# Performance work log

Measured on AMD Instinct MI355X. Metric: run time of the kernel, lower is better.

Reference implementation:

```python
import jax, jax.numpy as jnp
import numpy as np

DIM = 4096
N_HEADS = 32
N_KV = 8
HEAD_DIM = 128
BATCH = 32
CACHE_LEN = 2048 + 128  # hard-coded in init_kv_cache
START_POS = 2047
ROPE_BASE = 10000.0


def setup_inputs() -> dict:
    key = jax.random.key(0)
    ks = jax.random.split(key, 5)
    qkv_dim = (N_HEADS + 2 * N_KV) * HEAD_DIM  # fused QKV width
    return {
        "x": jax.random.normal(ks[0], (BATCH, DIM), jnp.float32) * 0.02,
        "wqkv": jax.random.normal(ks[1], (DIM, qkv_dim), jnp.float32) * 0.02,
        "wo": jax.random.normal(ks[2], (DIM, DIM), jnp.float32) * 0.02,
        "cache_k": jax.random.normal(ks[3], (BATCH, N_KV, CACHE_LEN, HEAD_DIM), jnp.float32) * 0.02,
        "cache_v": jax.random.normal(ks[4], (BATCH, N_KV, CACHE_LEN, HEAD_DIM), jnp.float32) * 0.02,
        "start_pos": START_POS,
    }


def _rope_cos_sin(pos):
    # Llama half-split RoPE; equivalent to the head_dim x head_dim rotation matrix
    half = HEAD_DIM // 2
    inv_freq = 1.0 / (ROPE_BASE ** (jnp.arange(half, dtype=jnp.float32) * 2.0 / HEAD_DIM))
    ang = pos * inv_freq
    cos = jnp.concatenate([jnp.cos(ang), jnp.cos(ang)])
    sin = jnp.concatenate([jnp.sin(ang), jnp.sin(ang)])
    return cos, sin


def _rotate_half(t):
    h = t.shape[-1] // 2
    return jnp.concatenate([-t[..., h:], t[..., :h]], axis=-1)


def reference(x, wqkv, wo, cache_k, cache_v, start_pos):
    scale = 1.0 / np.sqrt(HEAD_DIM)
    n_rep = N_HEADS // N_KV

    # fused QKV projection
    qkv = x @ wqkv  # (B, (H + 2*K) * D)
    q = qkv[:, : N_HEADS * HEAD_DIM].reshape(BATCH, N_KV, n_rep, HEAD_DIM)
    k = qkv[:, N_HEADS * HEAD_DIM : (N_HEADS + N_KV) * HEAD_DIM].reshape(BATCH, N_KV, HEAD_DIM)
    v = qkv[:, (N_HEADS + N_KV) * HEAD_DIM :].reshape(BATCH, N_KV, HEAD_DIM)

    # RoPE at position start_pos (rotation-matrix form in the original)
    cos, sin = _rope_cos_sin(jnp.float32(start_pos))
    q = q * cos + _rotate_half(q) * sin
    k = k * cos + _rotate_half(k) * sin

    # KV cache update at start_pos
    cache_k = cache_k.at[:, :, start_pos, :].set(k)
    cache_v = cache_v.at[:, :, start_pos, :].set(v)

    # grouped-query attention over the whole (masked) cache
    scores = jnp.einsum("bgrd,bgsd->bgrs", q, cache_k) * scale  # (B, KV, rep, S)
    valid = jnp.arange(CACHE_LEN) <= start_pos
    scores = jnp.where(valid[None, None, None, :], scores, jnp.float32(-1e9))
    probs = jax.nn.softmax(scores, axis=-1)
    attn = jnp.einsum("bgrs,bgsd->bgrd", probs, cache_v).reshape(BATCH, DIM)

    # output projection
    return attn @ wo
```

## Files before the change

### kernel.cpp

```cpp
#include <hip/hip_runtime.h>
#include <math.h>

#define DIM 4096
#define NH 32
#define NKV 8
#define HD 128
#define BATCH 32
#define CL 2176
#define QKV_DIM 6144
#define NREP 4

template<int N>
__global__ __launch_bounds__(256) void gemm_partial(const float* __restrict__ x,
                                                    const float* __restrict__ w,
                                                    float* __restrict__ part) {
    const int t = threadIdx.x;
    const int n0 = blockIdx.x * 256;
    const int k0 = blockIdx.y * 128;

    float acc[32];
#pragma unroll
    for (int b = 0; b < 32; ++b) acc[b] = 0.f;

    const float* wp = w + (size_t)k0 * N + n0 + t;
    const float* xp = x + k0;

    for (int kk = 0; kk < 128; kk += 4) {
        const float wv0 = wp[(size_t)(kk + 0) * N];
        const float wv1 = wp[(size_t)(kk + 1) * N];
        const float wv2 = wp[(size_t)(kk + 2) * N];
        const float wv3 = wp[(size_t)(kk + 3) * N];
#pragma unroll
        for (int b = 0; b < 32; ++b) {
            const float4 xv = *(const float4*)(xp + (size_t)b * DIM + kk);
            acc[b] = fmaf(xv.x, wv0, acc[b]);
            acc[b] = fmaf(xv.y, wv1, acc[b]);
            acc[b] = fmaf(xv.z, wv2, acc[b]);
            acc[b] = fmaf(xv.w, wv3, acc[b]);
        }
    }

    float* pp = part + (size_t)blockIdx.y * 32 * N + n0 + t;
#pragma unroll
    for (int b = 0; b < 32; ++b) pp[(size_t)b * N] = acc[b];
}

__global__ void qkv_finish(const float* __restrict__ part, const int* __restrict__ sp_p,
                           float* __restrict__ fin) {
    const int b = blockIdx.x, h = blockIdx.y, d = threadIdx.x;
    const int sp = *sp_p;
    const int col = h * 128 + d;

    float s = 0.f;
    for (int kc = 0; kc < 32; ++kc)
        s += part[(size_t)kc * 32 * QKV_DIM + (size_t)b * QKV_DIM + col];

    __shared__ float v[128];
    float outv = s;
    if (h < 40) {
        v[d] = s;
        __syncthreads();
        int j = d & 63;
        float inv_freq = powf(10000.0f, -(float)(2 * j) / 128.0f);
        float ang = (float)sp * inv_freq;
        float c = cosf(ang), sn = sinf(ang);
        float rot = (d < 64) ? -v[d + 64] : v[d - 64];
        outv = s * c + rot * sn;
    }
    fin[((size_t)b * 48 + h) * 128 + d] = outv;
}

__global__ __launch_bounds__(1024) void attn_scores(const float* __restrict__ fin,
                                                    const float* __restrict__ cache_k,
                                                    const int* __restrict__ sp_p,
                                                    float* __restrict__ scores) {
    const int bg = blockIdx.x;
    const int b = bg >> 3, g = bg & 7;
    const int sp = *sp_p;
    const int t = threadIdx.x;
    const int w = t >> 6, lane = t & 63, sl = lane & 31, half = lane >> 5;

    float4 qf[4];
#pragma unroll
    for (int h = 0; h < 4; ++h)
        qf[h] = *(const float4*)(fin + ((size_t)b * 48 + g * 4 + h) * 128 + sl * 4);

    const float scale = 0.08838834764831845f;
    const float* kbase = cache_k + ((size_t)b * NKV + g) * CL * HD;
    const float* knew = fin + ((size_t)b * 48 + 32 + g) * 128;

    const int s_begin = blockIdx.y * 1088;
    const int s_end = s_begin + 1088;

    for (int i = s_begin + w * 2; i < s_end; i += 32) {
        int s = i + half;
        if (i > sp) {
            if (sl == 0)
                *(float4*)(scores + ((size_t)bg * CL + s) * 4) =
                    make_float4(-1e9f, -1e9f, -1e9f, -1e9f);
            continue;
        }
        const float* krow = (s == sp) ? knew : (kbase + (size_t)s * HD);
        float4 kv = *(const float4*)(krow + sl * 4);

        float p[4];
#pragma unroll
        for (int h = 0; h < 4; ++h)
            p[h] = qf[h].x * kv.x + qf[h].y * kv.y + qf[h].z * kv.z + qf[h].w * kv.w;

#pragma unroll
        for (int off = 1; off < 32; off <<= 1) {
#pragma unroll
            for (int h = 0; h < 4; ++h) p[h] += __shfl_xor(p[h], off);
        }

        if (sl == 0) {
            bool valid = (s <= sp);
            float4 sc;
            sc.x = valid ? p[0] * scale : -1e9f;
            sc.y = valid ? p[1] * scale : -1e9f;
            sc.z = valid ? p[2] * scale : -1e9f;
            sc.w = valid ? p[3] * scale : -1e9f;
            *(float4*)(scores + ((size_t)bg * CL + s) * 4) = sc;
        }
    }
}

__global__ __launch_bounds__(1024) void attn_sm_pv(const float* __restrict__ scores,
                                                   const float* __restrict__ cache_v,
                                                   const float* __restrict__ fin,
                                                   const int* __restrict__ sp_p,
                                                   float* __restrict__ attn) {
    const int bg = blockIdx.x;
    const int b = bg >> 3, g = bg & 7;
    const int sp = *sp_p;
    const int t = threadIdx.x;
    const int w = t >> 6, lane = t & 63;
    const int grp = t >> 5, sl = t & 31, half = (t >> 5) & 1;

    __shared__ float smem[CL * 4];
    __shared__ float redw[16 * 4];
    __shared__ float redl[16 * 4];
    __shared__ float s_inv[4];

    const float* sb = scores + (size_t)bg * CL * 4;
    float4 vals[3];
    float m[4] = {-1e30f, -1e30f, -1e30f, -1e30f};
#pragma unroll
    for (int i = 0; i < 3; ++i) {
        int s = t + i * 1024;
        vals[i] = (s < CL) ? *(const float4*)(sb + (size_t)s * 4)
                           : make_float4(-1e30f, -1e30f, -1e30f, -1e30f);
        m[0] = fmaxf(m[0], vals[i].x);
        m[1] = fmaxf(m[1], vals[i].y);
        m[2] = fmaxf(m[2], vals[i].z);
        m[3] = fmaxf(m[3], vals[i].w);
    }
#pragma unroll
    for (int off = 1; off < 64; off <<= 1) {
#pragma unroll
        for (int h = 0; h < 4; ++h) m[h] = fmaxf(m[h], __shfl_xor(m[h], off));
    }
    if (lane == 0) {
#pragma unroll
        for (int h = 0; h < 4; ++h) redw[w * 4 + h] = m[h];
    }
    __syncthreads();
#pragma unroll
    for (int h = 0; h < 4; ++h) {
        float mm = redw[h];
        for (int ww = 1; ww < 16; ++ww) mm = fmaxf(mm, redw[ww * 4 + h]);
        m[h] = mm;
    }

    float l[4] = {0.f, 0.f, 0.f, 0.f};
#pragma unroll
    for (int i = 0; i < 3; ++i) {
        int s = t + i * 1024;
        if (s < CL) {
            float4 e;
            e.x = expf(vals[i].x - m[0]);
            e.y = expf(vals[i].y - m[1]);
            e.z = expf(vals[i].z - m[2]);
            e.w = expf(vals[i].w - m[3]);
            *(float4*)&smem[(size_t)s * 4] = e;
            l[0] += e.x; l[1] += e.y; l[2] += e.z; l[3] += e.w;
        }
    }
#pragma unroll
    for (int off = 1; off < 64; off <<= 1) {
#pragma unroll
        for (int h = 0; h < 4; ++h) l[h] += __shfl_xor(l[h], off);
    }
    if (lane == 0) {
#pragma unroll
        for (int h = 0; h < 4; ++h) redl[w * 4 + h] = l[h];
    }
    __syncthreads();
#pragma unroll
    for (int h = 0; h < 4; ++h) {
        float ll = redl[h];
        for (int ww = 1; ww < 16; ++ww) ll += redl[ww * 4 + h];
        l[h] = ll;
    }
    if (t == 0) {
        s_inv[0] = 1.f / l[0];
        s_inv[1] = 1.f / l[1];
        s_inv[2] = 1.f / l[2];
        s_inv[3] = 1.f / l[3];
    }

    const float* vbase = cache_v + ((size_t)b * NKV + g) * CL * HD;
    const float* vnew = fin + ((size_t)b * 48 + 40 + g) * 128;

    float o[4][4];
#pragma unroll
    for (int h = 0; h < 4; ++h)
#pragma unroll
        for (int c = 0; c < 4; ++c) o[h][c] = 0.f;

    for (int s = grp; s <= sp; s += 32) {
        const float* vrow = (s == sp) ? vnew : (vbase + (size_t)s * HD);
        float4 vv = *(const float4*)(vrow + sl * 4);
        float4 pp = *(const float4*)&smem[(size_t)s * 4];
        o[0][0] += pp.x * vv.x; o[0][1] += pp.x * vv.y; o[0][2] += pp.x * vv.z; o[0][3] += pp.x * vv.w;
        o[1][0] += pp.y * vv.x; o[1][1] += pp.y * vv.y; o[1][2] += pp.y * vv.z; o[1][3] += pp.y * vv.w;
        o[2][0] += pp.z * vv.x; o[2][1] += pp.z * vv.y; o[2][2] += pp.z * vv.z; o[2][3] += pp.z * vv.w;
        o[3][0] += pp.w * vv.x; o[3][1] += pp.w * vv.y; o[3][2] += pp.w * vv.z; o[3][3] += pp.w * vv.w;
    }

#pragma unroll
    for (int h = 0; h < 4; ++h)
#pragma unroll
        for (int c = 0; c < 4; ++c) o[h][c] += __shfl_xor(o[h][c], 32);

    __syncthreads();

    if (half == 0) {
#pragma unroll
        for (int h = 0; h < 4; ++h)
            *(float4*)&smem[w * 512 + h * 128 + sl * 4] =
                make_float4(o[h][0], o[h][1], o[h][2], o[h][3]);
    }
    __syncthreads();

    for (int step = 8; step >= 1; step >>= 1) {
        if (w < step) {
#pragma unroll
            for (int i = 0; i < 8; ++i) {
                int j = lane + i * 64;
                smem[w * 512 + j] += smem[(w + step) * 512 + j];
            }
        }
        __syncthreads();
    }

    if (t < 512) {
        int h = t >> 7, d = t & 127;
        attn[(size_t)b * DIM + (g * 4 + h) * 128 + d] = smem[h * 128 + d] * s_inv[h];
    }
}

__global__ void out_reduce(const float* __restrict__ part, float* __restrict__ out) {
    const int e = blockIdx.x * 256 + threadIdx.x;
    float s = 0.f;
    for (int kc = 0; kc < 32; ++kc) s += part[(size_t)kc * 32 * DIM + e];
    out[e] = s;
}

extern "C" void kernel_launch(void* const* d_in, const int* in_sizes, int n_in,
                              void* d_out, int out_size, void* d_ws, size_t ws_size,
                              hipStream_t stream) {
    const float* x       = (const float*)d_in[0];
    const float* wqkv    = (const float*)d_in[1];
    const float* wo      = (const float*)d_in[2];
    const float* cache_k = (const float*)d_in[3];
    const float* cache_v = (const float*)d_in[4];
    const int*   sp      = (const int*)d_in[5];
    float* out = (float*)d_out;
    float* ws  = (float*)d_ws;

    float* part1  = ws;
    float* fin    = part1 + 6291456;
    float* scores = fin + 196608;
    float* attn   = scores + 2228224;
    float* part2  = attn + 131072;

    gemm_partial<QKV_DIM><<<dim3(24, 32), 256, 0, stream>>>(x, wqkv, part1);
    qkv_finish<<<dim3(32, 48), 128, 0, stream>>>(part1, sp, fin);
    attn_scores<<<dim3(256, 2), 1024, 0, stream>>>(fin, cache_k, sp, scores);
    attn_sm_pv<<<256, 1024, 0, stream>>>(scores, cache_v, fin, sp, attn);
    gemm_partial<DIM><<<dim3(16, 32), 256, 0, stream>>>(attn, wo, part2);
    out_reduce<<<512, 256, 0, stream>>>(part2, out);
}
```

Before: 741.3 us.

## Fuse QKV reduction, RoPE, scores, softmax and PV into one attention kernel

Replaces the qkv_finish, attn_scores and attn_sm_pv kernels with a single attn_fused kernel per (batch, kv-group). The new kernel reduces the QKV partial sums and applies RoPE in shared memory, computes scores directly into a shared buffer, then runs softmax and the PV product. This removes two launches and the global round-trips for the fin and scores buffers. The K scan changes from a warp-cooperative dot product to one thread per cache row, which leaves global loads across a wavefront strided by a full row and may put more pressure on the caches.

```diff
diff --git a/kernel.cpp b/kernel.cpp
--- a/kernel.cpp
+++ b/kernel.cpp
@@ -45,90 +45,9 @@
     for (int b = 0; b < 32; ++b) pp[(size_t)b * N] = acc[b];
 }
 
-__global__ void qkv_finish(const float* __restrict__ part, const int* __restrict__ sp_p,
-                           float* __restrict__ fin) {
-    const int b = blockIdx.x, h = blockIdx.y, d = threadIdx.x;
-    const int sp = *sp_p;
-    const int col = h * 128 + d;
-
-    float s = 0.f;
-    for (int kc = 0; kc < 32; ++kc)
-        s += part[(size_t)kc * 32 * QKV_DIM + (size_t)b * QKV_DIM + col];
-
-    __shared__ float v[128];
-    float outv = s;
-    if (h < 40) {
-        v[d] = s;
-        __syncthreads();
-        int j = d & 63;
-        float inv_freq = powf(10000.0f, -(float)(2 * j) / 128.0f);
-        float ang = (float)sp * inv_freq;
-        float c = cosf(ang), sn = sinf(ang);
-        float rot = (d < 64) ? -v[d + 64] : v[d - 64];
-        outv = s * c + rot * sn;
-    }
-    fin[((size_t)b * 48 + h) * 128 + d] = outv;
-}
-
-__global__ __launch_bounds__(1024) void attn_scores(const float* __restrict__ fin,
-                                                    const float* __restrict__ cache_k,
-                                                    const int* __restrict__ sp_p,
-                                                    float* __restrict__ scores) {
-    const int bg = blockIdx.x;
-    const int b = bg >> 3, g = bg & 7;
-    const int sp = *sp_p;
-    const int t = threadIdx.x;
-    const int w = t >> 6, lane = t & 63, sl = lane & 31, half = lane >> 5;
-
-    float4 qf[4];
-#pragma unroll
-    for (int h = 0; h < 4; ++h)
-        qf[h] = *(const float4*)(fin + ((size_t)b * 48 + g * 4 + h) * 128 + sl * 4);
-
-    const float scale = 0.08838834764831845f;
-    const float* kbase = cache_k + ((size_t)b * NKV + g) * CL * HD;
-    const float* knew = fin + ((size_t)b * 48 + 32 + g) * 128;
-
-    const int s_begin = blockIdx.y * 1088;
-    const int s_end = s_begin + 1088;
-
-    for (int i = s_begin + w * 2; i < s_end; i += 32) {
-        int s = i + half;
-        if (i > sp) {
-            if (sl == 0)
-                *(float4*)(scores + ((size_t)bg * CL + s) * 4) =
-                    make_float4(-1e9f, -1e9f, -1e9f, -1e9f);
-            continue;
-        }
-        const float* krow = (s == sp) ? knew : (kbase + (size_t)s * HD);
-        float4 kv = *(const float4*)(krow + sl * 4);
-
-        float p[4];
-#pragma unroll
-        for (int h = 0; h < 4; ++h)
-            p[h] = qf[h].x * kv.x + qf[h].y * kv.y + qf[h].z * kv.z + qf[h].w * kv.w;
-
-#pragma unroll
-        for (int off = 1; off < 32; off <<= 1) {
-#pragma unroll
-            for (int h = 0; h < 4; ++h) p[h] += __shfl_xor(p[h], off);
-        }
-
-        if (sl == 0) {
-            bool valid = (s <= sp);
-            float4 sc;
-            sc.x = valid ? p[0] * scale : -1e9f;
-            sc.y = valid ? p[1] * scale : -1e9f;
-            sc.z = valid ? p[2] * scale : -1e9f;
-            sc.w = valid ? p[3] * scale : -1e9f;
-            *(float4*)(scores + ((size_t)bg * CL + s) * 4) = sc;
-        }
-    }
-}
-
-__global__ __launch_bounds__(1024) void attn_sm_pv(const float* __restrict__ scores,
+__global__ __launch_bounds__(1024) void attn_fused(const float* __restrict__ part,
+                                                   const float* __restrict__ cache_k,
                                                    const float* __restrict__ cache_v,
-                                                   const float* __restrict__ fin,
                                                    const int* __restrict__ sp_p,
                                                    float* __restrict__ attn) {
     const int bg = blockIdx.x;
@@ -136,25 +55,95 @@
     const int sp = *sp_p;
     const int t = threadIdx.x;
     const int w = t >> 6, lane = t & 63;
-    const int grp = t >> 5, sl = t & 31, half = (t >> 5) & 1;
-
-    __shared__ float smem[CL * 4];
-    __shared__ float redw[16 * 4];
+    const int grp = t >> 5, sl = t & 31, half = grp & 1;
+
+    __shared__ float sc[CL * 4];
+    __shared__ float q_s[4 * HD];
+    __shared__ float k_s[HD];
+    __shared__ float v_s[HD];
+    __shared__ float raw[6 * HD];
+    __shared__ float redm[16 * 4];
     __shared__ float redl[16 * 4];
     __shared__ float s_inv[4];
 
-    const float* sb = scores + (size_t)bg * CL * 4;
-    float4 vals[3];
+    const float scale = 0.08838834764831845f;
+
+    if (t < 768) {
+        const int hl = t >> 7, d = t & 127;
+        int col;
+        if (hl < 4)       col = g * 512 + t;
+        else if (hl == 4) col = 4096 + g * 128 + d;
+        else              col = 5120 + g * 128 + d;
+        const float* pp = part + (size_t)b * QKV_DIM + col;
+        float s = 0.f;
+        for (int kc = 0; kc < 32; ++kc)
+            s += pp[(size_t)kc * 32 * QKV_DIM];
+        raw[t] = s;
+    }
+    __syncthreads();
+    if (t < 768) {
+        const int hl = t >> 7, d = t & 127;
+        float s = raw[t];
+        float outv = s;
+        if (hl < 5) {
+            int j = d & 63;
+            float inv_freq = powf(10000.0f, -(float)(2 * j) / 128.0f);
+            float ang = (float)sp * inv_freq;
+            float c = cosf(ang), sn = sinf(ang);
+            int base = t & ~127;
+            float rot = (d < 64) ? -raw[base + d + 64] : raw[base + d - 64];
+            outv = s * c + rot * sn;
+        }
+        if (hl < 4)       q_s[t] = outv * scale;
+        else if (hl == 4) k_s[d] = outv;
+        else              v_s[d] = outv;
+    }
+    __syncthreads();
+
+    const float* kbase = cache_k + ((size_t)b * NKV + g) * (size_t)CL * HD;
+    for (int sA = t; sA < sp; sA += 2048) {
+        const int sB = sA + 1024;
+        const bool hasB = (sB < sp);
+        const float* krA = kbase + (size_t)sA * HD;
+        const float* krB = kbase + (size_t)sB * HD;
+        float pA0 = 0.f, pA1 = 0.f, pA2 = 0.f, pA3 = 0.f;
+        float pB0 = 0.f, pB1 = 0.f, pB2 = 0.f, pB3 = 0.f;
+#pragma unroll 4
+        for (int kk = 0; kk < HD; kk += 4) {
+            const float4 q0 = *(const float4*)&q_s[0 * HD + kk];
+            const float4 q1 = *(const float4*)&q_s[1 * HD + kk];
+            const float4 q2 = *(const float4*)&q_s[2 * HD + kk];
+            const float4 q3 = *(const float4*)&q_s[3 * HD + kk];
+            const float4 ka = *(const float4*)(krA + kk);
+            pA0 += q0.x * ka.x + q0.y * ka.y + q0.z * ka.z + q0.w * ka.w;
+            pA1 += q1.x * ka.x + q1.y * ka.y + q1.z * ka.z + q1.w * ka.w;
+            pA2 += q2.x * ka.x + q2.y * ka.y + q2.z * ka.z + q2.w * ka.w;
+            pA3 += q3.x * ka.x + q3.y * ka.y + q3.z * ka.z + q3.w * ka.w;
+            if (hasB) {
+                const float4 kb = *(const float4*)(krB + kk);
+                pB0 += q0.x * kb.x + q0.y * kb.y + q0.z * kb.z + q0.w * kb.w;
+                pB1 += q1.x * kb.x + q1.y * kb.y + q1.z * kb.z + q1.w * kb.w;
+                pB2 += q2.x * kb.x + q2.y * kb.y + q2.z * kb.z + q2.w * kb.w;
+                pB3 += q3.x * kb.x + q3.y * kb.y + q3.z * kb.z + q3.w * kb.w;
+            }
+        }
+        *(float4*)&sc[(size_t)sA * 4] = make_float4(pA0, pA1, pA2, pA3);
+        if (hasB) *(float4*)&sc[(size_t)sB * 4] = make_float4(pB0, pB1, pB2, pB3);
+    }
+    if (t < 4) {
+        float p = 0.f;
+        for (int k = 0; k < HD; ++k) p += q_s[t * HD + k] * k_s[k];
+        sc[(size_t)sp * 4 + t] = p;
+    }
+    __syncthreads();
+
     float m[4] = {-1e30f, -1e30f, -1e30f, -1e30f};
-#pragma unroll
-    for (int i = 0; i < 3; ++i) {
-        int s = t + i * 1024;
-        vals[i] = (s < CL) ? *(const float4*)(sb + (size_t)s * 4)
-                           : make_float4(-1e30f, -1e30f, -1e30f, -1e30f);
-        m[0] = fmaxf(m[0], vals[i].x);
-        m[1] = fmaxf(m[1], vals[i].y);
-        m[2] = fmaxf(m[2], vals[i].z);
-        m[3] = fmaxf(m[3], vals[i].w);
+    for (int s = t; s <= sp; s += 1024) {
+        const float4 v = *(const float4*)&sc[(size_t)s * 4];
+        m[0] = fmaxf(m[0], v.x);
+        m[1] = fmaxf(m[1], v.y);
+        m[2] = fmaxf(m[2], v.z);
+        m[3] = fmaxf(m[3], v.w);
     }
 #pragma unroll
     for (int off = 1; off < 64; off <<= 1) {
@@ -163,29 +152,25 @@
     }
     if (lane == 0) {
 #pragma unroll
-        for (int h = 0; h < 4; ++h) redw[w * 4 + h] = m[h];
+        for (int h = 0; h < 4; ++h) redm[w * 4 + h] = m[h];
     }
     __syncthreads();
 #pragma unroll
     for (int h = 0; h < 4; ++h) {
-        float mm = redw[h];
-        for (int ww = 1; ww < 16; ++ww) mm = fmaxf(mm, redw[ww * 4 + h]);
+        float mm = redm[h];
+        for (int ww = 1; ww < 16; ++ww) mm = fmaxf(mm, redm[ww * 4 + h]);
         m[h] = mm;
     }
 
     float l[4] = {0.f, 0.f, 0.f, 0.f};
-#pragma unroll
-    for (int i = 0; i < 3; ++i) {
-        int s = t + i * 1024;
-        if (s < CL) {
-            float4 e;
-            e.x = expf(vals[i].x - m[0]);
-            e.y = expf(vals[i].y - m[1]);
-            e.z = expf(vals[i].z - m[2]);
-            e.w = expf(vals[i].w - m[3]);
-            *(float4*)&smem[(size_t)s * 4] = e;
-            l[0] += e.x; l[1] += e.y; l[2] += e.z; l[3] += e.w;
-        }
+    for (int s = t; s <= sp; s += 1024) {
+        float4 v = *(const float4*)&sc[(size_t)s * 4];
+        v.x = expf(v.x - m[0]);
+        v.y = expf(v.y - m[1]);
+        v.z = expf(v.z - m[2]);
+        v.w = expf(v.w - m[3]);
+        *(float4*)&sc[(size_t)s * 4] = v;
+        l[0] += v.x; l[1] += v.y; l[2] += v.z; l[3] += v.w;
     }
 #pragma unroll
     for (int off = 1; off < 64; off <<= 1) {
@@ -197,37 +182,39 @@
         for (int h = 0; h < 4; ++h) redl[w * 4 + h] = l[h];
     }
     __syncthreads();
-#pragma unroll
-    for (int h = 0; h < 4; ++h) {
-        float ll = redl[h];
-        for (int ww = 1; ww < 16; ++ww) ll += redl[ww * 4 + h];
-        l[h] = ll;
-    }
     if (t == 0) {
-        s_inv[0] = 1.f / l[0];
-        s_inv[1] = 1.f / l[1];
-        s_inv[2] = 1.f / l[2];
-        s_inv[3] = 1.f / l[3];
-    }
-
-    const float* vbase = cache_v + ((size_t)b * NKV + g) * CL * HD;
-    const float* vnew = fin + ((size_t)b * 48 + 40 + g) * 128;
-
+        float l0 = 0.f, l1 = 0.f, l2 = 0.f, l3 = 0.f;
+        for (int ww = 0; ww < 16; ++ww) {
+            l0 += redl[ww * 4 + 0]; l1 += redl[ww * 4 + 1];
+            l2 += redl[ww * 4 + 2]; l3 += redl[ww * 4 + 3];
+        }
+        s_inv[0] = 1.f / l0; s_inv[1] = 1.f / l1;
+        s_inv[2] = 1.f / l2; s_inv[3] = 1.f / l3;
+    }
+
+    const float* vbase = cache_v + ((size_t)b * NKV + g) * (size_t)CL * HD;
     float o[4][4];
 #pragma unroll
     for (int h = 0; h < 4; ++h)
 #pragma unroll
         for (int c = 0; c < 4; ++c) o[h][c] = 0.f;
 
-    for (int s = grp; s <= sp; s += 32) {
-        const float* vrow = (s == sp) ? vnew : (vbase + (size_t)s * HD);
-        float4 vv = *(const float4*)(vrow + sl * 4);
-        float4 pp = *(const float4*)&smem[(size_t)s * 4];
+    for (int s = grp; s < sp; s += 32) {
+        const float4 vv = *(const float4*)(vbase + (size_t)s * HD + sl * 4);
+        const float4 pp = *(const float4*)&sc[(size_t)s * 4];
         o[0][0] += pp.x * vv.x; o[0][1] += pp.x * vv.y; o[0][2] += pp.x * vv.z; o[0][3] += pp.x * vv.w;
         o[1][0] += pp.y * vv.x; o[1][1] += pp.y * vv.y; o[1][2] += pp.y * vv.z; o[1][3] += pp.y * vv.w;
         o[2][0] += pp.z * vv.x; o[2][1] += pp.z * vv.y; o[2][2] += pp.z * vv.z; o[2][3] += pp.z * vv.w;
         o[3][0] += pp.w * vv.x; o[3][1] += pp.w * vv.y; o[3][2] += pp.w * vv.z; o[3][3] += pp.w * vv.w;
     }
+    if ((sp & 31) == grp) {
+        const float4 pp = *(const float4*)&sc[(size_t)sp * 4];
+        const float4 vv = *(const float4*)&v_s[sl * 4];
+        o[0][0] += pp.x * vv.x; o[0][1] += pp.x * vv.y; o[0][2] += pp.x * vv.z; o[0][3] += pp.x * vv.w;
+        o[1][0] += pp.y * vv.x; o[1][1] += pp.y * vv.y; o[1][2] += pp.y * vv.z; o[1][3] += pp.y * vv.w;
+        o[2][0] += pp.z * vv.x; o[2][1] += pp.z * vv.y; o[2][2] += pp.z * vv.z; o[2][3] += pp.z * vv.w;
+        o[3][0] += pp.w * vv.x; o[3][1] += pp.w * vv.y; o[3][2] += pp.w * vv.z; o[3][3] += pp.w * vv.w;
+    }
 
 #pragma unroll
     for (int h = 0; h < 4; ++h)
@@ -239,7 +226,7 @@
     if (half == 0) {
 #pragma unroll
         for (int h = 0; h < 4; ++h)
-            *(float4*)&smem[w * 512 + h * 128 + sl * 4] =
+            *(float4*)&sc[w * 512 + h * 128 + sl * 4] =
                 make_float4(o[h][0], o[h][1], o[h][2], o[h][3]);
     }
     __syncthreads();
@@ -249,7 +236,7 @@
 #pragma unroll
             for (int i = 0; i < 8; ++i) {
                 int j = lane + i * 64;
-                smem[w * 512 + j] += smem[(w + step) * 512 + j];
+                sc[w * 512 + j] += sc[(w + step) * 512 + j];
             }
         }
         __syncthreads();
@@ -257,7 +244,7 @@
 
     if (t < 512) {
         int h = t >> 7, d = t & 127;
-        attn[(size_t)b * DIM + (g * 4 + h) * 128 + d] = smem[h * 128 + d] * s_inv[h];
+        attn[(size_t)b * DIM + (g * 4 + h) * 128 + d] = sc[h * 128 + d] * s_inv[h];
     }
 }
 
@@ -281,15 +268,11 @@
     float* ws  = (float*)d_ws;
 
     float* part1  = ws;
-    float* fin    = part1 + 6291456;
-    float* scores = fin + 196608;
-    float* attn   = scores + 2228224;
+    float* attn   = part1 + 6291456;
     float* part2  = attn + 131072;
 
     gemm_partial<QKV_DIM><<<dim3(24, 32), 256, 0, stream>>>(x, wqkv, part1);
-    qkv_finish<<<dim3(32, 48), 128, 0, stream>>>(part1, sp, fin);
-    attn_scores<<<dim3(256, 2), 1024, 0, stream>>>(fin, cache_k, sp, scores);
-    attn_sm_pv<<<256, 1024, 0, stream>>>(scores, cache_v, fin, sp, attn);
+    attn_fused<<<256, 1024, 0, stream>>>(part1, cache_k, cache_v, sp, attn);
     gemm_partial<DIM><<<dim3(16, 32), 256, 0, stream>>>(attn, wo, part2);
     out_reduce<<<512, 256, 0, stream>>>(part2, out);
 }
```

Result: slower. 928.4 us (+25.2%).
